# Optimization experiments

Hardware: AMD Instinct MI355X
Metric: run time of the kernel (lower is better)

## Reference

```python
import jax, jax.numpy as jnp
import numpy as np

B, S, D_IN, D_OUT = 4, 2048, 1024, 1024
N_TREES, DEPTH, N_HEADS = 12, 3, 3
N_INTERNAL = 2 ** DEPTH - 1  # 7
N_LEAVES = 2 ** DEPTH        # 8
TEMPERATURE = 1.0
SOFTPLUS_SHIFT = 0.5413      # softplus(0.5413) ~= 1.0, so init node temp ~ 1


def _build_path_indices(depth):
    """Root-to-leaf internal-node indices and go-left directions per leaf."""
    L = 2 ** depth
    pi = np.zeros((L, depth), np.int32)
    pd = np.zeros((L, depth), np.float32)
    for leaf in range(L):
        node = 0
        for d in range(depth):
            pi[leaf, d] = node
            bit = (leaf >> (depth - 1 - d)) & 1
            pd[leaf, d] = 1.0 - bit
            node = 2 * node + 1 + bit
    return pi, pd


def setup_inputs() -> dict:
    key = jax.random.key(0)
    ks = jax.random.split(key, 4)
    x = jax.random.normal(ks[0], (B, S, D_IN), dtype=jnp.float32)
    # normal(0, 0.1) routing init
    decision_weights = 0.1 * jax.random.normal(ks[1], (N_TREES, N_INTERNAL, D_IN), dtype=jnp.float32)
    decision_biases = jnp.zeros((N_TREES, N_INTERNAL), dtype=jnp.float32)
    node_temperature_logits = jnp.zeros((N_TREES, N_INTERNAL), dtype=jnp.float32)
    # nn.Linear default init ~ U(-1/sqrt(D), 1/sqrt(D)); use matching-scale normal
    gate_w = jax.random.normal(ks[2], (N_TREES, D_IN), dtype=jnp.float32) / np.sqrt(D_IN)
    gate_b = jnp.zeros((N_TREES,), dtype=jnp.float32)
    # xavier_normal over each [n_leaves, output_dim] slice
    xav_std = np.sqrt(2.0 / (N_LEAVES + D_OUT))
    leaf_outputs = xav_std * jax.random.normal(ks[3], (N_HEADS, N_TREES, N_LEAVES, D_OUT), dtype=jnp.float32)
    pi, pd = _build_path_indices(DEPTH)
    return {
        "x": x,
        "decision_weights": decision_weights,
        "decision_biases": decision_biases,
        "node_temperature_logits": node_temperature_logits,
        "gate_w": gate_w,
        "gate_b": gate_b,
        "leaf_outputs": leaf_outputs,
        "path_indices": jnp.asarray(pi),
        "path_dirs": jnp.asarray(pd),
    }


def reference(x, decision_weights, decision_biases, node_temperature_logits,
              gate_w, gate_b, leaf_outputs, path_indices, path_dirs):
    # decisions: [B, S, T, N_internal]
    decisions = jnp.einsum('bsd,tnd->bstn', x, decision_weights) + decision_biases
    node_temps = TEMPERATURE * jax.nn.softplus(node_temperature_logits + SOFTPLUS_SHIFT)
    decisions = jax.nn.sigmoid(decisions / node_temps)
    # gather nodes along each root->leaf path: [B, S, T, L, depth]
    relevant = decisions[..., path_indices]
    probs_per_level = path_dirs * relevant + (1.0 - path_dirs) * (1.0 - relevant)
    leaf_probs = probs_per_level.prod(axis=-1)  # [B, S, T, L]
    # softmax gate over trees: [B, S, T]
    weights = jax.nn.softmax(jnp.einsum('bsd,td->bst', x, gate_w) + gate_b, axis=-1)
    # fold tree gate into leaf probs, then contract leaves against leaf outputs
    routed = leaf_probs * weights[..., None]            # [B, S, T, L]
    out = jnp.einsum('bstl,htld->hbsd', routed, leaf_outputs)  # [H, B, S, Dout]
    return out
```

## Files before the change

### kernel.cpp

```cpp
#include <hip/hip_runtime.h>

typedef __attribute__((ext_vector_type(8))) short short8;
typedef __attribute__((ext_vector_type(4))) float floatx4;
typedef unsigned int uint;
typedef unsigned short ushort;
typedef __attribute__((ext_vector_type(4))) uint uintx4;

#define NTOK   8192
#define DIN    1024
#define DOUT   1024
#define NJ     96
#define TOKPB  16
#define XSTR   136
#define DSTR   97
#define SSTR   85
#define RSTR   104
#define LOT_H  (DOUT * NJ)

static __device__ inline ushort f2b(float f) {
    uint u = __builtin_bit_cast(uint, f);
    u = u + 0x7fffu + ((u >> 16) & 1u);
    return (ushort)(u >> 16);
}
static __device__ inline uint pack2(float a, float b) {
    return (uint)f2b(a) | ((uint)f2b(b) << 16);
}

__global__ __launch_bounds__(256) void k_prep(const float* __restrict__ lo,
                                              const float* __restrict__ dw,
                                              const float* __restrict__ gw,
                                              ushort* __restrict__ lot,
                                              ushort* __restrict__ wcat) {
    int i = blockIdx.x * 256 + threadIdx.x;
    if (i < 3 * LOT_H) {
        int h = i / LOT_H;
        int rem = i - h * LOT_H;
        int k = rem >> 10;
        int d = rem & 1023;
        lot[h * LOT_H + d * NJ + k] = f2b(lo[i]);
    } else {
        int j = i - 3 * LOT_H;
        int r = j >> 10, c = j & 1023;
        float v = (r < 84) ? dw[r * DIN + c] : gw[(r - 84) * DIN + c];
        wcat[j] = f2b(v);
    }
}

__global__ __launch_bounds__(256, 2) void k_fused(
    const float* __restrict__ x,
    const ushort* __restrict__ wcat,
    const float* __restrict__ db,
    const float* __restrict__ ntl,
    const float* __restrict__ gb,
    const int*   __restrict__ pi,
    const float* __restrict__ pd,
    const ushort* __restrict__ lot,
    float* __restrict__ out)
{
    __shared__ __attribute__((aligned(16))) char smem[30464];
    __shared__ __attribute__((aligned(16))) ushort rt[TOKPB][RSTR];
    __shared__ float invt[84];
    __shared__ float biasf[96];
    __shared__ int   pis[24];
    __shared__ float pds[24];

    ushort* xl = (ushort*)smem;
    ushort* wl = (ushort*)(smem + TOKPB * XSTR * 2);
    float*  decis = (float*)smem;
    float*  sdecs = (float*)(smem + TOKPB * DSTR * 4);

    const int tid = threadIdx.x;
    const int tb  = blockIdx.x * TOKPB;

    if (tid < 84) {
        float z = ntl[tid] + 0.5413f;
        float sp = (z > 20.0f) ? z : log1pf(__expf(z));
        invt[tid]  = 1.0f / sp;
        biasf[tid] = db[tid];
    } else if (tid < 96) {
        biasf[tid] = gb[tid - 84];
    } else if (tid < 120) {
        pis[tid - 96] = pi[tid - 96];
    } else if (tid < 144) {
        pds[tid - 120] = pd[tid - 120];
    }

    const int wave = tid >> 6, lane = tid & 63;
    const int lrow = lane & 15, quad = lane >> 4;

    const int nt0 = wave;
    const bool two = (wave < 2);
    const int nt1 = wave + 4;

    floatx4 acc0 = (floatx4)(0.0f), acc1 = (floatx4)(0.0f);

    floatx4 xv[2][2];
    uintx4  wv[2][6];

#define LOADX(B, KC) do { \
    _Pragma("unroll") for (int i_ = 0; i_ < 2; ++i_) { \
        int idx_ = tid + 256 * i_; \
        int r_ = idx_ >> 5, c_ = idx_ & 31; \
        xv[B][i_] = __builtin_nontemporal_load( \
            (const floatx4*)(x + (size_t)(tb + r_) * DIN + (KC) * 128 + c_ * 4)); \
    } } while (0)

#define LOADW(B, KC) do { \
    _Pragma("unroll") for (int i_ = 0; i_ < 6; ++i_) { \
        int idx_ = tid + 256 * i_; \
        int r_ = idx_ >> 4, c_ = idx_ & 15; \
        wv[B][i_] = *(const uintx4*)(wcat + r_ * DIN + (KC) * 128 + c_ * 8); \
    } } while (0)

#define STAGE(B) do { \
    _Pragma("unroll") for (int i_ = 0; i_ < 2; ++i_) { \
        int idx_ = tid + 256 * i_; \
        int r_ = idx_ >> 5, c_ = idx_ & 31; \
        uint2 p_; \
        p_.x = pack2(xv[B][i_][0], xv[B][i_][1]); \
        p_.y = pack2(xv[B][i_][2], xv[B][i_][3]); \
        *(uint2*)(xl + r_ * XSTR + c_ * 4) = p_; \
    } \
    _Pragma("unroll") for (int i_ = 0; i_ < 6; ++i_) { \
        int idx_ = tid + 256 * i_; \
        int r_ = idx_ >> 4, c_ = idx_ & 15; \
        *(uintx4*)(wl + r_ * XSTR + c_ * 8) = wv[B][i_]; \
    } } while (0)

    LOADX(0, 0);
    LOADW(0, 0);

#pragma unroll
    for (int kc = 0; kc < 8; ++kc) {
        const int cur = kc & 1, nxt = cur ^ 1;
        __syncthreads();
        STAGE(cur);
        __syncthreads();
        if (kc < 7) {
            LOADX(nxt, kc + 1);
            LOADW(nxt, kc + 1);
        }

        short8 a[4];
#pragma unroll
        for (int kt = 0; kt < 4; ++kt)
            a[kt] = *(const short8*)(xl + lrow * XSTR + kt * 32 + quad * 8);
#pragma unroll
        for (int kt = 0; kt < 4; ++kt) {
            short8 b0 = *(const short8*)(wl + (nt0 * 16 + lrow) * XSTR + kt * 32 + quad * 8);
            acc0 = __builtin_amdgcn_mfma_f32_16x16x32_bf16(a[kt], b0, acc0, 0, 0, 0);
        }
        if (two) {
#pragma unroll
            for (int kt = 0; kt < 4; ++kt) {
                short8 b1 = *(const short8*)(wl + (nt1 * 16 + lrow) * XSTR + kt * 32 + quad * 8);
                acc1 = __builtin_amdgcn_mfma_f32_16x16x32_bf16(a[kt], b1, acc1, 0, 0, 0);
            }
        }
    }
#undef LOADX
#undef LOADW
#undef STAGE

    __syncthreads();
#pragma unroll
    for (int r = 0; r < 4; ++r)
        decis[(quad * 4 + r) * DSTR + nt0 * 16 + lrow] = acc0[r];
    if (two) {
#pragma unroll
        for (int r = 0; r < 4; ++r)
            decis[(quad * 4 + r) * DSTR + nt1 * 16 + lrow] = acc1[r];
    }
    __syncthreads();

#pragma unroll
    for (int i = 0; i < 6; ++i) {
        int idx = tid + 256 * i;
        if (idx < TOKPB * 84) {
            int tk = idx / 84, nd = idx - tk * 84;
            float dv = (decis[tk * DSTR + nd] + biasf[nd]) * invt[nd];
            sdecs[tk * SSTR + nd] = 1.0f / (1.0f + __expf(-dv));
        }
    }
    __syncthreads();

    {
        const int tk = tid >> 4, l = (tid >> 1) & 7, th = tid & 1;
        float g[12], gm = -1e30f;
#pragma unroll
        for (int tt = 0; tt < 12; ++tt) {
            g[tt] = decis[tk * DSTR + 84 + tt] + biasf[84 + tt];
            gm = fmaxf(gm, g[tt]);
        }
        float gs = 0.0f;
#pragma unroll
        for (int tt = 0; tt < 12; ++tt) { g[tt] = __expf(g[tt] - gm); gs += g[tt]; }
        float ginv = 1.0f / gs;

        const int   n0 = pis[l * 3 + 0], n1 = pis[l * 3 + 1], n2 = pis[l * 3 + 2];
        const float d0 = pds[l * 3 + 0], d1 = pds[l * 3 + 1], d2 = pds[l * 3 + 2];
        const float* sd = sdecs + tk * SSTR;
        const int t0 = th * 6;
#pragma unroll
        for (int t = 0; t < 6; ++t) {
            int tt = t0 + t;
            float s0 = sd[tt * 7 + n0], s1 = sd[tt * 7 + n1], s2 = sd[tt * 7 + n2];
            float pb = g[tt] * ginv
                     * (d0 * s0 + (1.0f - d0) * (1.0f - s0))
                     * (d1 * s1 + (1.0f - d1) * (1.0f - s1))
                     * (d2 * s2 + (1.0f - d2) * (1.0f - s2));
            rt[tk][tt * 8 + l] = f2b(pb);
        }
    }
    __syncthreads();

    {
        short8 a[3];
#pragma unroll
        for (int kk = 0; kk < 3; ++kk)
            a[kk] = *(const short8*)(&rt[lrow][quad * 8 + kk * 32]);

        short8 bb[3][6];
#define LOADB(B, G) do { \
    _Pragma("unroll") for (int q_ = 0; q_ < 2; ++q_) { \
        int c_ = wave * 768 + ((G) * 2 + q_) * 16; \
        int h_ = c_ >> 10; \
        int d_ = (c_ & 1023) + lrow; \
        const ushort* bp_ = lot + (size_t)h_ * LOT_H + (size_t)d_ * NJ + quad * 8; \
        _Pragma("unroll") for (int kk_ = 0; kk_ < 3; ++kk_) \
            bb[B][q_ * 3 + kk_] = *(const short8*)(bp_ + kk_ * 32); \
    } } while (0)

        LOADB(0, 0);
        LOADB(1, 1);
#pragma unroll
        for (int g = 0; g < 24; ++g) {
            const int cur = g % 3;
            if (g < 22) LOADB((g + 2) % 3, g + 2);
#pragma unroll
            for (int q = 0; q < 2; ++q) {
                floatx4 c0 = (floatx4)(0.0f);
#pragma unroll
                for (int kk = 0; kk < 3; ++kk)
                    c0 = __builtin_amdgcn_mfma_f32_16x16x32_bf16(a[kk], bb[cur][q * 3 + kk], c0, 0, 0, 0);
                int c = wave * 768 + (g * 2 + q) * 16;
                int h = c >> 10;
                int d = (c & 1023) + lrow;
                float* ob = out + ((size_t)h * NTOK + tb) * DOUT + d;
#pragma unroll
                for (int r = 0; r < 4; ++r)
                    __builtin_nontemporal_store(c0[r], ob + (size_t)(quad * 4 + r) * DOUT);
            }
        }
#undef LOADB
    }
}

extern "C" void kernel_launch(void* const* d_in, const int* in_sizes, int n_in,
                              void* d_out, int out_size, void* d_ws, size_t ws_size,
                              hipStream_t stream) {
    const float* x   = (const float*)d_in[0];
    const float* dw  = (const float*)d_in[1];
    const float* db  = (const float*)d_in[2];
    const float* ntl = (const float*)d_in[3];
    const float* gw  = (const float*)d_in[4];
    const float* gb  = (const float*)d_in[5];
    const float* lo  = (const float*)d_in[6];
    const int*   pi  = (const int*)d_in[7];
    const float* pd  = (const float*)d_in[8];
    float* out = (float*)d_out;

    ushort* lot  = (ushort*)d_ws;
    ushort* wcat = lot + (size_t)3 * LOT_H;

    k_prep<<<dim3((3 * LOT_H + NJ * DIN) / 256), dim3(256), 0, stream>>>(lo, dw, gw, lot, wcat);
    k_fused<<<dim3(NTOK / TOKPB), dim3(256), 0, stream>>>(x, wcat, db, ntl, gb, pi, pd, lot, out);
}
```

Before: 162.7 us.

## Load MFMA operands directly from global memory, dropping LDS staging

The decision GEMM no longer stages x and the concatenated weights through shared memory with double-buffered register prefetch and block barriers. Each wave instead reads its MFMA fragments straight from global memory and converts x to bf16 in registers. This removes two barriers per K chunk and shrinks shared memory. In exchange, each wave re-reads and re-converts the same x rows, accesses are less coalesced, and the nontemporal hint is lost.

```diff
diff --git a/kernel.cpp b/kernel.cpp
--- a/kernel.cpp
+++ b/kernel.cpp
@@ -11,7 +11,6 @@
 #define DOUT   1024
 #define NJ     96
 #define TOKPB  16
-#define XSTR   136
 #define DSTR   97
 #define SSTR   85
 #define RSTR   104
@@ -57,17 +56,13 @@
     const ushort* __restrict__ lot,
     float* __restrict__ out)
 {
-    __shared__ __attribute__((aligned(16))) char smem[30464];
+    __shared__ float decis[TOKPB * DSTR];
+    __shared__ float sdecs[TOKPB * SSTR];
     __shared__ __attribute__((aligned(16))) ushort rt[TOKPB][RSTR];
     __shared__ float invt[84];
     __shared__ float biasf[96];
     __shared__ int   pis[24];
     __shared__ float pds[24];
-
-    ushort* xl = (ushort*)smem;
-    ushort* wl = (ushort*)(smem + TOKPB * XSTR * 2);
-    float*  decis = (float*)smem;
-    float*  sdecs = (float*)(smem + TOKPB * DSTR * 4);
 
     const int tid = threadIdx.x;
     const int tb  = blockIdx.x * TOKPB;
@@ -94,75 +89,38 @@
 
     floatx4 acc0 = (floatx4)(0.0f), acc1 = (floatx4)(0.0f);
 
-    floatx4 xv[2][2];
-    uintx4  wv[2][6];
-
-#define LOADX(B, KC) do { \
-    _Pragma("unroll") for (int i_ = 0; i_ < 2; ++i_) { \
-        int idx_ = tid + 256 * i_; \
-        int r_ = idx_ >> 5, c_ = idx_ & 31; \
-        xv[B][i_] = __builtin_nontemporal_load( \
-            (const floatx4*)(x + (size_t)(tb + r_) * DIN + (KC) * 128 + c_ * 4)); \
-    } } while (0)
-
-#define LOADW(B, KC) do { \
-    _Pragma("unroll") for (int i_ = 0; i_ < 6; ++i_) { \
-        int idx_ = tid + 256 * i_; \
-        int r_ = idx_ >> 4, c_ = idx_ & 15; \
-        wv[B][i_] = *(const uintx4*)(wcat + r_ * DIN + (KC) * 128 + c_ * 8); \
-    } } while (0)
-
-#define STAGE(B) do { \
-    _Pragma("unroll") for (int i_ = 0; i_ < 2; ++i_) { \
-        int idx_ = tid + 256 * i_; \
-        int r_ = idx_ >> 5, c_ = idx_ & 31; \
-        uint2 p_; \
-        p_.x = pack2(xv[B][i_][0], xv[B][i_][1]); \
-        p_.y = pack2(xv[B][i_][2], xv[B][i_][3]); \
-        *(uint2*)(xl + r_ * XSTR + c_ * 4) = p_; \
-    } \
-    _Pragma("unroll") for (int i_ = 0; i_ < 6; ++i_) { \
-        int idx_ = tid + 256 * i_; \
-        int r_ = idx_ >> 4, c_ = idx_ & 15; \
-        *(uintx4*)(wl + r_ * XSTR + c_ * 8) = wv[B][i_]; \
-    } } while (0)
-
-    LOADX(0, 0);
-    LOADW(0, 0);
+    const float*  xr = x    + (size_t)(tb + lrow) * DIN + quad * 8;
+    const ushort* w0 = wcat + (size_t)(nt0 * 16 + lrow) * DIN + quad * 8;
+    const ushort* w1 = wcat + (size_t)(nt1 * 16 + lrow) * DIN + quad * 8;
 
 #pragma unroll
     for (int kc = 0; kc < 8; ++kc) {
-        const int cur = kc & 1, nxt = cur ^ 1;
-        __syncthreads();
-        STAGE(cur);
-        __syncthreads();
-        if (kc < 7) {
-            LOADX(nxt, kc + 1);
-            LOADW(nxt, kc + 1);
-        }
-
         short8 a[4];
 #pragma unroll
-        for (int kt = 0; kt < 4; ++kt)
-            a[kt] = *(const short8*)(xl + lrow * XSTR + kt * 32 + quad * 8);
-#pragma unroll
         for (int kt = 0; kt < 4; ++kt) {
-            short8 b0 = *(const short8*)(wl + (nt0 * 16 + lrow) * XSTR + kt * 32 + quad * 8);
+            floatx4 u = *(const floatx4*)(xr + kc * 128 + kt * 32);
+            floatx4 v = *(const floatx4*)(xr + kc * 128 + kt * 32 + 4);
+            union { short8 s; uint w[4]; } pk;
+            pk.w[0] = pack2(u[0], u[1]);
+            pk.w[1] = pack2(u[2], u[3]);
+            pk.w[2] = pack2(v[0], v[1]);
+            pk.w[3] = pack2(v[2], v[3]);
+            a[kt] = pk.s;
+        }
+#pragma unroll
+        for (int kt = 0; kt < 4; ++kt) {
+            short8 b0 = *(const short8*)(w0 + kc * 128 + kt * 32);
             acc0 = __builtin_amdgcn_mfma_f32_16x16x32_bf16(a[kt], b0, acc0, 0, 0, 0);
         }
         if (two) {
 #pragma unroll
             for (int kt = 0; kt < 4; ++kt) {
-                short8 b1 = *(const short8*)(wl + (nt1 * 16 + lrow) * XSTR + kt * 32 + quad * 8);
+                short8 b1 = *(const short8*)(w1 + kc * 128 + kt * 32);
                 acc1 = __builtin_amdgcn_mfma_f32_16x16x32_bf16(a[kt], b1, acc1, 0, 0, 0);
             }
         }
     }
-#undef LOADX
-#undef LOADW
-#undef STAGE
-
-    __syncthreads();
+
 #pragma unroll
     for (int r = 0; r < 4; ++r)
         decis[(quad * 4 + r) * DSTR + nt0 * 16 + lrow] = acc0[r];
```

Measured after the change: 173.5 us. 1.07x slower.

## Tile leaf-output layout for contiguous B loads and swap MFMA operands for vector stores

Applied to the files above, without the earlier changes.

The bf16 leaf-output table is re-laid out into 16x32 tiles so each wave's B-fragment loads come from contiguous 512-element blocks instead of rows strided by NJ. The MFMA operands are swapped so each lane's accumulator holds four consecutive output columns of one token, which allows a single 16-byte store in place of four scalar nontemporal stores. This aims to cut uncoalesced global reads and the cost of the output write stream. The nontemporal store hint is dropped in exchange.

```diff
diff --git a/kernel.cpp b/kernel.cpp
--- a/kernel.cpp
+++ b/kernel.cpp
@@ -37,7 +37,8 @@
         int rem = i - h * LOT_H;
         int k = rem >> 10;
         int d = rem & 1023;
-        lot[h * LOT_H + d * NJ + k] = f2b(lo[i]);
+        int off = (((d >> 4) * 3 + (k >> 5)) << 9) + ((d & 15) << 5) + (k & 31);
+        lot[h * LOT_H + off] = f2b(lo[i]);
     } else {
         int j = i - 3 * LOT_H;
         int r = j >> 10, c = j & 1023;
@@ -215,20 +216,23 @@
     __syncthreads();
 
     {
-        short8 a[3];
+        short8 ar[3];
 #pragma unroll
         for (int kk = 0; kk < 3; ++kk)
-            a[kk] = *(const short8*)(&rt[lrow][quad * 8 + kk * 32]);
-
+            ar[kk] = *(const short8*)(&rt[lrow][quad * 8 + kk * 32]);
+
+        const int tilebase = wave * 48;
         short8 bb[3][6];
 #define LOADB(B, G) do { \
     _Pragma("unroll") for (int q_ = 0; q_ < 2; ++q_) { \
-        int c_ = wave * 768 + ((G) * 2 + q_) * 16; \
-        int h_ = c_ >> 10; \
-        int d_ = (c_ & 1023) + lrow; \
-        const ushort* bp_ = lot + (size_t)h_ * LOT_H + (size_t)d_ * NJ + quad * 8; \
-        _Pragma("unroll") for (int kk_ = 0; kk_ < 3; ++kk_) \
-            bb[B][q_ * 3 + kk_] = *(const short8*)(bp_ + kk_ * 32); \
+        int t_ = tilebase + (G) * 2 + q_; \
+        int h_ = t_ >> 6; \
+        int dt_ = t_ & 63; \
+        const ushort* p_ = lot + (size_t)h_ * LOT_H + dt_ * 1536 \
+                         + (lrow << 5) + quad * 8; \
+        bb[B][q_ * 3 + 0] = *(const short8*)(p_); \
+        bb[B][q_ * 3 + 1] = *(const short8*)(p_ + 512); \
+        bb[B][q_ * 3 + 2] = *(const short8*)(p_ + 1024); \
     } } while (0)
 
         LOADB(0, 0);
@@ -239,17 +243,14 @@
             if (g < 22) LOADB((g + 2) % 3, g + 2);
 #pragma unroll
             for (int q = 0; q < 2; ++q) {
-                floatx4 c0 = (floatx4)(0.0f);
+                floatx4 c = (floatx4)(0.0f);
 #pragma unroll
                 for (int kk = 0; kk < 3; ++kk)
-                    c0 = __builtin_amdgcn_mfma_f32_16x16x32_bf16(a[kk], bb[cur][q * 3 + kk], c0, 0, 0, 0);
-                int c = wave * 768 + (g * 2 + q) * 16;
-                int h = c >> 10;
-                int d = (c & 1023) + lrow;
-                float* ob = out + ((size_t)h * NTOK + tb) * DOUT + d;
-#pragma unroll
-                for (int r = 0; r < 4; ++r)
-                    __builtin_nontemporal_store(c0[r], ob + (size_t)(quad * 4 + r) * DOUT);
+                    c = __builtin_amdgcn_mfma_f32_16x16x32_bf16(bb[cur][q * 3 + kk], ar[kk], c, 0, 0, 0);
+                const int t = tilebase + g * 2 + q;
+                const int h = t >> 6;
+                const int d = (t & 63) * 16 + quad * 4;
+                *(floatx4*)(out + ((size_t)h * NTOK + tb + lrow) * DOUT + d) = c;
             }
         }
 #undef LOADB
```

Result: faster. 157.9 us (-3.0%).
